# Kernel optimization log

Hardware: AMD Instinct MI355X
Metric: run time of the kernel (lower is better)

The kernel has to match this reference:

```python
import jax, jax.numpy as jnp
import numpy as np

N = 8_388_608
T_MAX = 4096


def setup_inputs() -> dict:
    key = jax.random.key(0)
    k1, k2, k3 = jax.random.split(key, 3)
    risk = jax.random.normal(k1, (N,), dtype=jnp.float32)
    time = jax.random.randint(k2, (N,), 0, T_MAX, dtype=jnp.int64)
    event = jax.random.randint(k3, (N,), 0, 2, dtype=jnp.int64)
    return {"risk": risk, "time": time, "event": event}


def reference(risk, time, event):
    # Sort descending by time (matches torch.argsort(time, descending=True)).
    order = jnp.argsort(-time)
    r = risk[order]            # [N] risk sorted by descending time
    t = time[order]            # [N]
    e = event[order] > 0       # [N] bool

    n = r.shape[0]
    # Cumulative (prefix) logsumexp over descending-sorted risks.
    # At-risk set for time t is exactly the prefix ending at the LAST index
    # of t's tie group, so log_denom(group) = clse[last_idx_of_group].
    clse = jax.lax.associative_scan(jnp.logaddexp, r)  # [N]

    # Last index of each contiguous tie block (times equal => contiguous after sort).
    is_last = jnp.concatenate([t[:-1] != t[1:], jnp.ones((1,), dtype=bool)])
    idx = jnp.arange(n)
    cand = jnp.where(is_last, idx, n)          # non-last positions -> sentinel
    last_idx = jax.lax.cummin(cand, axis=0, reverse=True)  # min over j >= i

    log_denom = clse[last_idx]                 # [N] per-sample group denominator

    # nll = -sum_groups(sum_{events in group} risk  -  d_group * log_denom)
    #     =  sum_{i: event_i} (log_denom_i - risk_i)
    nll = jnp.sum(jnp.where(e, log_denom - r, jnp.float32(0.0)))

    has_events = jnp.sum(event > 0) > 0
    return jnp.where(has_events, nll, jnp.float32(0.0))
```

## Files before the change

### kernel.cpp

```cpp
#include <hip/hip_runtime.h>

#define TMAX 4096
#define ABLOCKS 512
#define ATHREADS 1024
#define PERTHREAD_V4 4

#define SCALE_F 1048576.0f
#define INV_SCALE (1.0 / 1048576.0)
#define SUM_MASK 0xFFFFFFFFFFFFULL
#define CNT_SHIFT 48

#define RB 32
#define RS 32

__global__ __launch_bounds__(ATHREADS, 8) void coxph_hist_fixed(
    const float* __restrict__ risk, const int* __restrict__ time_,
    const int* __restrict__ event,
    float* __restrict__ psum, unsigned short* __restrict__ pcnt,
    float* __restrict__ pevr)
{
    __shared__ unsigned long long s_acc[TMAX];
    __shared__ float s_evr[ATHREADS / 64];

    const int tid = threadIdx.x;
    #pragma unroll
    for (int k = 0; k < TMAX / ATHREADS; ++k) s_acc[tid + k * ATHREADS] = 0ull;
    __syncthreads();

    const float4* r4 = (const float4*)risk;
    const int4*   t4 = (const int4*)time_;
    const int4*   e4 = (const int4*)event;

    const int base = blockIdx.x * ATHREADS + tid;
    const int STRIDE4 = ABLOCKS * ATHREADS;

    float4 r[PERTHREAD_V4]; int4 t[PERTHREAD_V4]; int4 e[PERTHREAD_V4];
    #pragma unroll
    for (int k = 0; k < PERTHREAD_V4; ++k) {
        const int i = base + k * STRIDE4;
        r[k] = r4[i]; t[k] = t4[i]; e[k] = e4[i];
    }

    float evr = 0.f;
    #pragma unroll
    for (int k = 0; k < PERTHREAD_V4; ++k) {
        {
            unsigned long long pk =
                (unsigned long long)(__expf(r[k].x) * SCALE_F + 0.5f)
                | ((unsigned long long)(unsigned)e[k].x << CNT_SHIFT);
            atomicAdd(&s_acc[t[k].x & (TMAX - 1)], pk);
            evr += e[k].x ? r[k].x : 0.f;
        }
        {
            unsigned long long pk =
                (unsigned long long)(__expf(r[k].y) * SCALE_F + 0.5f)
                | ((unsigned long long)(unsigned)e[k].y << CNT_SHIFT);
            atomicAdd(&s_acc[t[k].y & (TMAX - 1)], pk);
            evr += e[k].y ? r[k].y : 0.f;
        }
        {
            unsigned long long pk =
                (unsigned long long)(__expf(r[k].z) * SCALE_F + 0.5f)
                | ((unsigned long long)(unsigned)e[k].z << CNT_SHIFT);
            atomicAdd(&s_acc[t[k].z & (TMAX - 1)], pk);
            evr += e[k].z ? r[k].z : 0.f;
        }
        {
            unsigned long long pk =
                (unsigned long long)(__expf(r[k].w) * SCALE_F + 0.5f)
                | ((unsigned long long)(unsigned)e[k].w << CNT_SHIFT);
            atomicAdd(&s_acc[t[k].w & (TMAX - 1)], pk);
            evr += e[k].w ? r[k].w : 0.f;
        }
    }

    #pragma unroll
    for (int off = 32; off > 0; off >>= 1) evr += __shfl_down(evr, off);
    const int lane = tid & 63, wave = tid >> 6;
    if (lane == 0) s_evr[wave] = evr;
    __syncthreads();

    float*          ps = psum + (size_t)blockIdx.x * TMAX;
    unsigned short* pc = pcnt + (size_t)blockIdx.x * TMAX;
    #pragma unroll
    for (int k = 0; k < TMAX / ATHREADS; ++k) {
        const int i = tid + k * ATHREADS;
        unsigned long long v = s_acc[i];
        ps[i] = (float)((double)(v & SUM_MASK) * INV_SCALE);
        pc[i] = (unsigned short)(v >> CNT_SHIFT);
    }
    if (tid == 0) {
        float tot = 0.f;
        for (int w = 0; w < ATHREADS / 64; ++w) tot += s_evr[w];
        pevr[blockIdx.x] = tot;
    }
}

__global__ __launch_bounds__(ATHREADS, 8) void coxph_hist_generic(
    const float* __restrict__ risk, const int* __restrict__ time_,
    const int* __restrict__ event,
    float* __restrict__ psum, unsigned short* __restrict__ pcnt,
    float* __restrict__ pevr, int n)
{
    __shared__ unsigned long long s_acc[TMAX];
    __shared__ float s_evr[ATHREADS / 64];

    const int tid = threadIdx.x;
    #pragma unroll
    for (int k = 0; k < TMAX / ATHREADS; ++k) s_acc[tid + k * ATHREADS] = 0ull;
    __syncthreads();

    float evr = 0.f;
    const int stride = gridDim.x * ATHREADS;
    for (int i = blockIdx.x * ATHREADS + tid; i < n; i += stride) {
        float rv = risk[i];
        int   ev = event[i];
        unsigned long long pk =
            (unsigned long long)(__expf(rv) * SCALE_F + 0.5f)
            | ((unsigned long long)(unsigned)ev << CNT_SHIFT);
        atomicAdd(&s_acc[time_[i] & (TMAX - 1)], pk);
        evr += ev ? rv : 0.f;
    }

    #pragma unroll
    for (int off = 32; off > 0; off >>= 1) evr += __shfl_down(evr, off);
    const int lane = tid & 63, wave = tid >> 6;
    if (lane == 0) s_evr[wave] = evr;
    __syncthreads();

    float*          ps = psum + (size_t)blockIdx.x * TMAX;
    unsigned short* pc = pcnt + (size_t)blockIdx.x * TMAX;
    #pragma unroll
    for (int k = 0; k < TMAX / ATHREADS; ++k) {
        const int i = tid + k * ATHREADS;
        unsigned long long v = s_acc[i];
        ps[i] = (float)((double)(v & SUM_MASK) * INV_SCALE);
        pc[i] = (unsigned short)(v >> CNT_SHIFT);
    }
    if (tid == 0) {
        float tot = 0.f;
        for (int w = 0; w < ATHREADS / 64; ++w) tot += s_evr[w];
        pevr[blockIdx.x] = tot;
    }
}

__global__ __launch_bounds__(1024) void coxph_reduce(
    const float* __restrict__ psum, const unsigned short* __restrict__ pcnt,
    float* __restrict__ bsum, unsigned* __restrict__ bcnt)
{
    __shared__ float    ls[RS * RB];
    __shared__ unsigned lc[RS * RB];

    const int t = threadIdx.x;
    const int j = t & (RB - 1);
    const int s = t >> 5;
    const int bucket = blockIdx.x * RB + j;

    float sum = 0.f; unsigned cnt = 0u;
    #pragma unroll
    for (int k = 0; k < ABLOCKS / RS; ++k) {
        const int row = s * (ABLOCKS / RS) + k;
        sum += psum[(size_t)row * TMAX + bucket];
        cnt += pcnt[(size_t)row * TMAX + bucket];
    }
    ls[t] = sum; lc[t] = cnt;
    __syncthreads();

    #pragma unroll
    for (int h = RS / 2; h >= 1; h >>= 1) {
        if (s < h) { ls[t] += ls[t + h * RB]; lc[t] += lc[t + h * RB]; }
        __syncthreads();
    }
    if (s == 0) { bsum[bucket] = ls[j]; bcnt[bucket] = lc[j]; }
}

__global__ __launch_bounds__(1024) void coxph_finalize(
    const float* __restrict__ bsum, const unsigned* __restrict__ bcnt,
    const float* __restrict__ pevr, int nevr, float* __restrict__ out)
{
    __shared__ float    s_wsum[16];
    __shared__ double   s_dacc[16];
    __shared__ unsigned s_cacc[16];

    const int tid = threadIdx.x;
    const int lane = tid & 63, wave = tid >> 6;

    const int j0 = 4 * tid;
    float v0 = bsum[TMAX - 1 - j0];
    float v1 = bsum[TMAX - 2 - j0];
    float v2 = bsum[TMAX - 3 - j0];
    float v3 = bsum[TMAX - 4 - j0];
    float p0 = v0, p1 = p0 + v1, p2 = p1 + v2, p3 = p2 + v3;

    float t_incl = p3;
    #pragma unroll
    for (int off = 1; off < 64; off <<= 1) {
        float u = __shfl_up(t_incl, off);
        if (lane >= off) t_incl += u;
    }
    if (lane == 63) s_wsum[wave] = t_incl;
    __syncthreads();
    if (tid == 0) {
        float acc = 0.f;
        for (int w = 0; w < 16; ++w) { float x = s_wsum[w]; s_wsum[w] = acc; acc += x; }
    }
    __syncthreads();
    const float excl = (t_incl - p3) + s_wsum[wave];

    double acc = 0.0;
    unsigned ctot = 0u;
    unsigned c0 = bcnt[TMAX - 1 - j0];
    unsigned c1 = bcnt[TMAX - 2 - j0];
    unsigned c2 = bcnt[TMAX - 3 - j0];
    unsigned c3 = bcnt[TMAX - 4 - j0];
    if (c0) { acc += (double)c0 * (double)logf(excl + p0); ctot += c0; }
    if (c1) { acc += (double)c1 * (double)logf(excl + p1); ctot += c1; }
    if (c2) { acc += (double)c2 * (double)logf(excl + p2); ctot += c2; }
    if (c3) { acc += (double)c3 * (double)logf(excl + p3); ctot += c3; }

    if (tid < nevr) acc -= (double)pevr[tid];

    #pragma unroll
    for (int off = 32; off > 0; off >>= 1) {
        acc  += __shfl_down(acc, off);
        ctot += __shfl_down(ctot, off);
    }
    if (lane == 0) { s_dacc[wave] = acc; s_cacc[wave] = ctot; }
    __syncthreads();
    if (tid == 0) {
        double a = 0.0; unsigned c = 0u;
        for (int w = 0; w < 16; ++w) { a += s_dacc[w]; c += s_cacc[w]; }
        out[0] = c ? (float)a : 0.0f;
    }
}

extern "C" void kernel_launch(void* const* d_in, const int* in_sizes, int n_in,
                              void* d_out, int out_size, void* d_ws, size_t ws_size,
                              hipStream_t stream)
{
    const float* risk  = (const float*)d_in[0];
    const int*   time_ = (const int*)d_in[1];
    const int*   event = (const int*)d_in[2];
    float* out = (float*)d_out;
    const int n = in_sizes[0];

    char* ws = (char*)d_ws;
    const size_t psum_bytes = (size_t)ABLOCKS * TMAX * sizeof(float);
    const size_t pcnt_bytes = (size_t)ABLOCKS * TMAX * sizeof(unsigned short);
    size_t off = 0;
    float*          psum = (float*)(ws + off);          off += psum_bytes;
    unsigned short* pcnt = (unsigned short*)(ws + off); off += pcnt_bytes;
    float*          pevr = (float*)(ws + off);          off += ABLOCKS * sizeof(float);
    float*          bsum = (float*)(ws + off);          off += TMAX * sizeof(float);
    unsigned*       bcnt = (unsigned*)(ws + off);       off += TMAX * sizeof(unsigned);

    if (n == ABLOCKS * ATHREADS * 4 * PERTHREAD_V4) {
        coxph_hist_fixed<<<ABLOCKS, ATHREADS, 0, stream>>>(
            risk, time_, event, psum, pcnt, pevr);
    } else {
        coxph_hist_generic<<<ABLOCKS, ATHREADS, 0, stream>>>(
            risk, time_, event, psum, pcnt, pevr, n);
    }
    coxph_reduce<<<TMAX / RB, RS * RB, 0, stream>>>(psum, pcnt, bsum, bcnt);
    coxph_finalize<<<1, 1024, 0, stream>>>(bsum, bcnt, pevr, ABLOCKS, out);
}
```

Baseline: 127.1 us.

## Fuse reduce and finalize via last-block atomic counter and stagger histogram loads

```diff
diff --git a/kernel.cpp b/kernel.cpp
--- a/kernel.cpp
+++ b/kernel.cpp
@@ -13,16 +13,33 @@
 #define RB 32
 #define RS 32
 
+#define PROC1(rv, tv, ev)                                                     \
+    {                                                                         \
+        const unsigned pk32 = (unsigned)(__expf(rv) * SCALE_F + 0.5f);        \
+        const unsigned long long pk = (unsigned long long)pk32                \
+            | ((unsigned long long)(unsigned)(ev) << CNT_SHIFT);              \
+        atomicAdd(&s_acc[(tv) & (TMAX - 1)], pk);                             \
+        evr = __builtin_fmaf((float)(ev), (rv), evr);                         \
+    }
+
+#define PROC4(rr, tt, ee)                                                     \
+    PROC1((rr).x, (tt).x, (ee).x)                                             \
+    PROC1((rr).y, (tt).y, (ee).y)                                             \
+    PROC1((rr).z, (tt).z, (ee).z)                                             \
+    PROC1((rr).w, (tt).w, (ee).w)
+
 __global__ __launch_bounds__(ATHREADS, 8) void coxph_hist_fixed(
     const float* __restrict__ risk, const int* __restrict__ time_,
     const int* __restrict__ event,
     float* __restrict__ psum, unsigned short* __restrict__ pcnt,
-    float* __restrict__ pevr)
+    float* __restrict__ pevr, unsigned* __restrict__ done)
 {
     __shared__ unsigned long long s_acc[TMAX];
     __shared__ float s_evr[ATHREADS / 64];
 
     const int tid = threadIdx.x;
+    if (blockIdx.x == 0 && tid == 0) *done = 0u;
+
     #pragma unroll
     for (int k = 0; k < TMAX / ATHREADS; ++k) s_acc[tid + k * ATHREADS] = 0ull;
     __syncthreads();
@@ -32,47 +49,21 @@
     const int4*   e4 = (const int4*)event;
 
     const int base = blockIdx.x * ATHREADS + tid;
-    const int STRIDE4 = ABLOCKS * ATHREADS;
-
-    float4 r[PERTHREAD_V4]; int4 t[PERTHREAD_V4]; int4 e[PERTHREAD_V4];
-    #pragma unroll
-    for (int k = 0; k < PERTHREAD_V4; ++k) {
-        const int i = base + k * STRIDE4;
-        r[k] = r4[i]; t[k] = t4[i]; e[k] = e4[i];
-    }
+    const int S4   = ABLOCKS * ATHREADS;
 
     float evr = 0.f;
-    #pragma unroll
-    for (int k = 0; k < PERTHREAD_V4; ++k) {
-        {
-            unsigned long long pk =
-                (unsigned long long)(__expf(r[k].x) * SCALE_F + 0.5f)
-                | ((unsigned long long)(unsigned)e[k].x << CNT_SHIFT);
-            atomicAdd(&s_acc[t[k].x & (TMAX - 1)], pk);
-            evr += e[k].x ? r[k].x : 0.f;
-        }
-        {
-            unsigned long long pk =
-                (unsigned long long)(__expf(r[k].y) * SCALE_F + 0.5f)
-                | ((unsigned long long)(unsigned)e[k].y << CNT_SHIFT);
-            atomicAdd(&s_acc[t[k].y & (TMAX - 1)], pk);
-            evr += e[k].y ? r[k].y : 0.f;
-        }
-        {
-            unsigned long long pk =
-                (unsigned long long)(__expf(r[k].z) * SCALE_F + 0.5f)
-                | ((unsigned long long)(unsigned)e[k].z << CNT_SHIFT);
-            atomicAdd(&s_acc[t[k].z & (TMAX - 1)], pk);
-            evr += e[k].z ? r[k].z : 0.f;
-        }
-        {
-            unsigned long long pk =
-                (unsigned long long)(__expf(r[k].w) * SCALE_F + 0.5f)
-                | ((unsigned long long)(unsigned)e[k].w << CNT_SHIFT);
-            atomicAdd(&s_acc[t[k].w & (TMAX - 1)], pk);
-            evr += e[k].w ? r[k].w : 0.f;
-        }
-    }
+
+    float4 r0 = r4[base];          int4 t0 = t4[base];          int4 e0 = e4[base];
+    float4 r1 = r4[base + S4];     int4 t1 = t4[base + S4];     int4 e1 = e4[base + S4];
+
+    float4 r2 = r4[base + 2 * S4]; int4 t2 = t4[base + 2 * S4]; int4 e2 = e4[base + 2 * S4];
+    PROC4(r0, t0, e0)
+
+    float4 r3 = r4[base + 3 * S4]; int4 t3 = t4[base + 3 * S4]; int4 e3 = e4[base + 3 * S4];
+    PROC4(r1, t1, e1)
+
+    PROC4(r2, t2, e2)
+    PROC4(r3, t3, e3)
 
     #pragma unroll
     for (int off = 32; off > 0; off >>= 1) evr += __shfl_down(evr, off);
@@ -100,12 +91,14 @@
     const float* __restrict__ risk, const int* __restrict__ time_,
     const int* __restrict__ event,
     float* __restrict__ psum, unsigned short* __restrict__ pcnt,
-    float* __restrict__ pevr, int n)
+    float* __restrict__ pevr, unsigned* __restrict__ done, int n)
 {
     __shared__ unsigned long long s_acc[TMAX];
     __shared__ float s_evr[ATHREADS / 64];
 
     const int tid = threadIdx.x;
+    if (blockIdx.x == 0 && tid == 0) *done = 0u;
+
     #pragma unroll
     for (int k = 0; k < TMAX / ATHREADS; ++k) s_acc[tid + k * ATHREADS] = 0ull;
     __syncthreads();
@@ -115,11 +108,8 @@
     for (int i = blockIdx.x * ATHREADS + tid; i < n; i += stride) {
         float rv = risk[i];
         int   ev = event[i];
-        unsigned long long pk =
-            (unsigned long long)(__expf(rv) * SCALE_F + 0.5f)
-            | ((unsigned long long)(unsigned)ev << CNT_SHIFT);
-        atomicAdd(&s_acc[time_[i] & (TMAX - 1)], pk);
-        evr += ev ? rv : 0.f;
+        int   tv = time_[i];
+        PROC1(rv, tv, ev)
     }
 
     #pragma unroll
@@ -144,9 +134,11 @@
     }
 }
 
-__global__ __launch_bounds__(1024) void coxph_reduce(
+__global__ __launch_bounds__(1024) void coxph_reduce_final(
     const float* __restrict__ psum, const unsigned short* __restrict__ pcnt,
-    float* __restrict__ bsum, unsigned* __restrict__ bcnt)
+    const float* __restrict__ pevr, int nevr,
+    float* __restrict__ bsumR, unsigned* __restrict__ bcntR,
+    unsigned* __restrict__ done, float* __restrict__ out)
 {
     __shared__ float    ls[RS * RB];
     __shared__ unsigned lc[RS * RB];
@@ -171,26 +163,25 @@
         if (s < h) { ls[t] += ls[t + h * RB]; lc[t] += lc[t + h * RB]; }
         __syncthreads();
     }
-    if (s == 0) { bsum[bucket] = ls[j]; bcnt[bucket] = lc[j]; }
-}
-
-__global__ __launch_bounds__(1024) void coxph_finalize(
-    const float* __restrict__ bsum, const unsigned* __restrict__ bcnt,
-    const float* __restrict__ pevr, int nevr, float* __restrict__ out)
-{
+    if (s == 0) { bsumR[TMAX - 1 - bucket] = ls[j]; bcntR[TMAX - 1 - bucket] = lc[j]; }
+
+    __shared__ unsigned s_old;
+    __threadfence();
+    __syncthreads();
+    if (t == 0) s_old = atomicAdd(done, 1u);
+    __syncthreads();
+    if (s_old != (unsigned)(gridDim.x - 1)) return;
+    __threadfence();
+
     __shared__ float    s_wsum[16];
     __shared__ double   s_dacc[16];
     __shared__ unsigned s_cacc[16];
 
-    const int tid = threadIdx.x;
+    const int tid = t;
     const int lane = tid & 63, wave = tid >> 6;
 
-    const int j0 = 4 * tid;
-    float v0 = bsum[TMAX - 1 - j0];
-    float v1 = bsum[TMAX - 2 - j0];
-    float v2 = bsum[TMAX - 3 - j0];
-    float v3 = bsum[TMAX - 4 - j0];
-    float p0 = v0, p1 = p0 + v1, p2 = p1 + v2, p3 = p2 + v3;
+    float4 v = ((const float4*)bsumR)[tid];
+    float p0 = v.x, p1 = p0 + v.y, p2 = p1 + v.z, p3 = p2 + v.w;
 
     float t_incl = p3;
     #pragma unroll
@@ -201,22 +192,18 @@
     if (lane == 63) s_wsum[wave] = t_incl;
     __syncthreads();
     if (tid == 0) {
-        float acc = 0.f;
-        for (int w = 0; w < 16; ++w) { float x = s_wsum[w]; s_wsum[w] = acc; acc += x; }
+        float a = 0.f;
+        for (int w = 0; w < 16; ++w) { float x = s_wsum[w]; s_wsum[w] = a; a += x; }
     }
     __syncthreads();
     const float excl = (t_incl - p3) + s_wsum[wave];
 
-    double acc = 0.0;
-    unsigned ctot = 0u;
-    unsigned c0 = bcnt[TMAX - 1 - j0];
-    unsigned c1 = bcnt[TMAX - 2 - j0];
-    unsigned c2 = bcnt[TMAX - 3 - j0];
-    unsigned c3 = bcnt[TMAX - 4 - j0];
-    if (c0) { acc += (double)c0 * (double)logf(excl + p0); ctot += c0; }
-    if (c1) { acc += (double)c1 * (double)logf(excl + p1); ctot += c1; }
-    if (c2) { acc += (double)c2 * (double)logf(excl + p2); ctot += c2; }
-    if (c3) { acc += (double)c3 * (double)logf(excl + p3); ctot += c3; }
+    uint4 c = ((const uint4*)bcntR)[tid];
+    double acc = 0.0; unsigned ctot = 0u;
+    if (c.x) { acc += (double)c.x * (double)logf(excl + p0); ctot += c.x; }
+    if (c.y) { acc += (double)c.y * (double)logf(excl + p1); ctot += c.y; }
+    if (c.z) { acc += (double)c.z * (double)logf(excl + p2); ctot += c.z; }
+    if (c.w) { acc += (double)c.w * (double)logf(excl + p3); ctot += c.w; }
 
     if (tid < nevr) acc -= (double)pevr[tid];
 
@@ -228,9 +215,9 @@
     if (lane == 0) { s_dacc[wave] = acc; s_cacc[wave] = ctot; }
     __syncthreads();
     if (tid == 0) {
-        double a = 0.0; unsigned c = 0u;
-        for (int w = 0; w < 16; ++w) { a += s_dacc[w]; c += s_cacc[w]; }
-        out[0] = c ? (float)a : 0.0f;
+        double a = 0.0; unsigned cc = 0u;
+        for (int w = 0; w < 16; ++w) { a += s_dacc[w]; cc += s_cacc[w]; }
+        out[0] = cc ? (float)a : 0.0f;
     }
 }
 
@@ -248,19 +235,20 @@
     const size_t psum_bytes = (size_t)ABLOCKS * TMAX * sizeof(float);
     const size_t pcnt_bytes = (size_t)ABLOCKS * TMAX * sizeof(unsigned short);
     size_t off = 0;
-    float*          psum = (float*)(ws + off);          off += psum_bytes;
-    unsigned short* pcnt = (unsigned short*)(ws + off); off += pcnt_bytes;
-    float*          pevr = (float*)(ws + off);          off += ABLOCKS * sizeof(float);
-    float*          bsum = (float*)(ws + off);          off += TMAX * sizeof(float);
-    unsigned*       bcnt = (unsigned*)(ws + off);       off += TMAX * sizeof(unsigned);
+    float*          psum  = (float*)(ws + off);          off += psum_bytes;
+    unsigned short* pcnt  = (unsigned short*)(ws + off); off += pcnt_bytes;
+    float*          pevr  = (float*)(ws + off);          off += ABLOCKS * sizeof(float);
+    float*          bsumR = (float*)(ws + off);          off += TMAX * sizeof(float);
+    unsigned*       bcntR = (unsigned*)(ws + off);       off += TMAX * sizeof(unsigned);
+    unsigned*       done  = (unsigned*)(ws + off);       off += sizeof(unsigned);
 
     if (n == ABLOCKS * ATHREADS * 4 * PERTHREAD_V4) {
         coxph_hist_fixed<<<ABLOCKS, ATHREADS, 0, stream>>>(
-            risk, time_, event, psum, pcnt, pevr);
+            risk, time_, event, psum, pcnt, pevr, done);
     } else {
         coxph_hist_generic<<<ABLOCKS, ATHREADS, 0, stream>>>(
-            risk, time_, event, psum, pcnt, pevr, n);
-    }
-    coxph_reduce<<<TMAX / RB, RS * RB, 0, stream>>>(psum, pcnt, bsum, bcnt);
-    coxph_finalize<<<1, 1024, 0, stream>>>(bsum, bcnt, pevr, ABLOCKS, out);
-}
+            risk, time_, event, psum, pcnt, pevr, done, n);
+    }
+    coxph_reduce_final<<<TMAX / RB, RS * RB, 0, stream>>>(
+        psum, pcnt, pevr, ABLOCKS, bsumR, bcntR, done, out);
+}
```

New measurement: 159.1 us. 25.2% more time.
